# Kernel tuning notes

Measured on AMD Instinct MI355X. Metric: run time of the kernel, lower is better.

Reference implementation:

```python
import jax, jax.numpy as jnp
import numpy as np

DIM = 768
HEADS = 12
HEAD_DIM = DIM // HEADS
SCALE = HEAD_DIM ** -0.5


def setup_inputs() -> dict:
    key = jax.random.key(0)
    k1, k2, k3, k4 = jax.random.split(key, 4)
    x = jax.random.normal(k1, (1, 4096, DIM), dtype=jnp.float32)
    # qkv: Linear(dim, 3*dim), bias=False
    W_qkv = jax.random.normal(k2, (DIM, 3 * DIM), dtype=jnp.float32) * (DIM ** -0.5)
    # proj: Linear(dim, dim) with bias
    W_proj = jax.random.normal(k3, (DIM, DIM), dtype=jnp.float32) * (DIM ** -0.5)
    b_proj = jax.random.normal(k4, (DIM,), dtype=jnp.float32) * 0.01
    return {"x": x, "W_qkv": W_qkv, "W_proj": W_proj, "b_proj": b_proj}


def reference(x, W_qkv, W_proj, b_proj):
    b, n, d = x.shape
    qkv = x @ W_qkv                                  # [b, n, 3d]
    q, k, v = jnp.split(qkv, 3, axis=-1)             # each [b, n, d]
    # split heads: [b, n, (h hd)] -> [b, h, n, hd]
    def heads(t):
        return t.reshape(b, n, HEADS, HEAD_DIM).transpose(0, 2, 1, 3)
    q, k, v = heads(q) * SCALE, heads(k), heads(v)
    sim = jnp.einsum('bhid,bhjd->bhij', q, k)        # [b, h, n, n] -- full score matrix
    attn = jax.nn.softmax(sim, axis=-1)
    out = jnp.einsum('bhij,bhjd->bhid', attn, v)     # [b, h, n, hd]
    out = out.transpose(0, 2, 1, 3).reshape(b, n, d)  # merge heads
    return out @ W_proj + b_proj
```

## Files before the change

kernel.cpp:

```cpp
#include <hip/hip_runtime.h>
#include <math.h>

#define TOKENS 4096
#define DMODEL 768
#define NHEADS 12
#define HDIM   64
#define QKV_N  2304
#define ATTN_SCALE 0.125f
#define QSCALE_LOG2E (0.125f * 1.44269504088896340736f)

typedef __attribute__((ext_vector_type(8))) short bf16x8;
typedef __attribute__((ext_vector_type(4))) float floatx4;

__device__ __forceinline__ ushort f2bf(float f) {
    union { float f; unsigned u; } cv; cv.f = f;
    unsigned u = cv.u;
    u += 0x7fffu + ((u >> 16) & 1u);
    return (ushort)(u >> 16);
}

__device__ __forceinline__ unsigned cvt_pk_bf16(float a, float b) {
    unsigned r;
    asm("v_cvt_pk_bf16_f32 %0, %1, %2" : "=v"(r) : "v"(a), "v"(b));
    return r;
}

__device__ __forceinline__ void gl2lds16(const ushort* g, ushort* l) {
    __builtin_amdgcn_global_load_lds(
        (const __attribute__((address_space(1))) void*)g,
        (__attribute__((address_space(3))) void*)l, 16, 0, 0);
}

__device__ __forceinline__ bf16x8 frag(const ushort* ls, int row, int chunk) {
    return *(const bf16x8*)(ls + row * 64 + ((chunk ^ (row & 7)) * 8));
}

__global__ __launch_bounds__(256) void cvt_bf16_kernel(
    const float* __restrict__ in, ushort* __restrict__ out, int n4)
{
    const int i = blockIdx.x * 256 + threadIdx.x;
    if (i < n4) {
        const float4 v = ((const float4*)in)[i];
        ushort4 h;
        h.x = f2bf(v.x); h.y = f2bf(v.y); h.z = f2bf(v.z); h.w = f2bf(v.w);
        ((ushort4*)out)[i] = h;
    }
}

__global__ __launch_bounds__(256) void transpose_cvt_kernel(
    const float* __restrict__ in, ushort* __restrict__ out, int R, int C)
{
    __shared__ ushort tile[32][33];
    const int tx  = threadIdx.x & 31;
    const int ty8 = threadIdx.x >> 5;
    const int c0 = blockIdx.x * 32;
    const int r0 = blockIdx.y * 32;
    #pragma unroll
    for (int p = 0; p < 4; ++p) {
        const int r = ty8 + p * 8;
        tile[r][tx] = f2bf(in[(size_t)(r0 + r) * C + c0 + tx]);
    }
    __syncthreads();
    #pragma unroll
    for (int p = 0; p < 4; ++p) {
        const int c = ty8 + p * 8;
        out[(size_t)(c0 + c) * R + r0 + tx] = tile[tx][c];
    }
}

template<int NT>
__device__ __forceinline__ void gemm_body_async(
    const ushort* __restrict__ A, const ushort* __restrict__ Bt, int K,
    int m0, int n0, floatx4 acc[4][NT], ushort* ls)
{
    ushort* lsA = ls;
    ushort* lsB = ls + 8192;

    const int tid  = threadIdx.x;
    const int lane = tid & 63;
    const int wave = tid >> 6;
    const int wm = wave >> 1, wn = wave & 1;
    const int quad = lane >> 4, l16 = lane & 15;

    const int lrow = lane >> 3;
    const int csw  = ((lane & 7) ^ lrow) * 8;

    const ushort* gA = A  + (size_t)(m0 + wave * 32 + lrow) * K + csw;
    const ushort* gB = Bt + (size_t)(n0 + wave * NT * 8 + lrow) * K + csw;
    ushort* lA = lsA + (wave * 32) * 64;
    ushort* lB = lsB + (wave * NT * 8) * 64;

    for (int k0 = 0; k0 < K; k0 += 64) {
        __syncthreads();
        #pragma unroll
        for (int p = 0; p < 4; ++p)
            gl2lds16(gA + (size_t)p * 8 * K + k0, lA + p * 8 * 64);
        #pragma unroll
        for (int p = 0; p < NT; ++p)
            gl2lds16(gB + (size_t)p * 8 * K + k0, lB + p * 8 * 64);
        __syncthreads();

        #pragma unroll
        for (int ks = 0; ks < 2; ++ks) {
            bf16x8 af[4], bfr[NT];
            #pragma unroll
            for (int mt = 0; mt < 4; ++mt)
                af[mt] = frag(lsA, wm * 64 + mt * 16 + l16, ks * 4 + quad);
            #pragma unroll
            for (int nt = 0; nt < NT; ++nt)
                bfr[nt] = frag(lsB, wn * NT * 16 + nt * 16 + l16, ks * 4 + quad);
            #pragma unroll
            for (int mt = 0; mt < 4; ++mt)
                #pragma unroll
                for (int nt = 0; nt < NT; ++nt)
                    acc[mt][nt] = __builtin_amdgcn_mfma_f32_16x16x32_bf16(
                        af[mt], bfr[nt], acc[mt][nt], 0, 0, 0);
        }
    }
}

__global__ __launch_bounds__(256) void gemm_qkv_mfma(
    const ushort* __restrict__ Xb, const ushort* __restrict__ Wt,
    ushort* __restrict__ Qb, ushort* __restrict__ Kb, ushort* __restrict__ Vt)
{
    __shared__ __align__(16) ushort ls[16384];
    const int m0 = blockIdx.y * 128;
    const int n0 = blockIdx.x * 128;

    floatx4 acc[4][4] = {};
    gemm_body_async<4>(Xb, Wt, DMODEL, m0, n0, acc, ls);

    const int tid  = threadIdx.x;
    const int lane = tid & 63;
    const int wave = tid >> 6;
    const int wm = wave >> 1, wn = wave & 1;
    const int quad = lane >> 4, l16 = lane & 15;

    if (n0 < 2 * DMODEL) {
        const float scale = (n0 < DMODEL) ? QSCALE_LOG2E : 1.0f;
        ushort* outp = (n0 < DMODEL) ? Qb : Kb;
        const int colg = (n0 < DMODEL) ? n0 : n0 - DMODEL;
        #pragma unroll
        for (int p = 0; p < 2; ++p) {
            __syncthreads();
            if (wm == p) {
                #pragma unroll
                for (int mt = 0; mt < 4; ++mt)
                    #pragma unroll
                    for (int nt = 0; nt < 4; ++nt) {
                        const int row = mt * 16 + quad * 4;
                        const int col = wn * 64 + nt * 16 + l16;
                        #pragma unroll
                        for (int r = 0; r < 4; ++r)
                            ls[(row + r) * 136 + col] = f2bf(acc[mt][nt][r] * scale);
                    }
            }
            __syncthreads();
            #pragma unroll
            for (int p2 = 0; p2 < 4; ++p2) {
                const int row = (tid >> 4) + p2 * 16;
                const int c8  = (tid & 15) * 8;
                *(uint4*)(outp + (size_t)(m0 + p * 64 + row) * DMODEL + colg + c8) =
                    *(const uint4*)(ls + row * 136 + c8);
            }
        }
    } else {
        const int hd0 = n0 - 2 * DMODEL;
        #pragma unroll
        for (int p = 0; p < 2; ++p) {
            __syncthreads();
            if (wn == p) {
                #pragma unroll
                for (int mt = 0; mt < 4; ++mt)
                    #pragma unroll
                    for (int nt = 0; nt < 4; ++nt) {
                        const int hd  = nt * 16 + l16;
                        const int tok = wm * 64 + mt * 16 + quad * 4;
                        #pragma unroll
                        for (int r = 0; r < 4; ++r)
                            ls[hd * 136 + tok + r] = f2bf(acc[mt][nt][r]);
                    }
            }
            __syncthreads();
            #pragma unroll
            for (int p2 = 0; p2 < 4; ++p2) {
                const int row = (tid >> 4) + p2 * 16;
                const int c8  = (tid & 15) * 8;
                *(uint4*)(Vt + (size_t)(hd0 + p * 64 + row) * TOKENS + m0 + c8) =
                    *(const uint4*)(ls + row * 136 + c8);
            }
        }
    }
}

__global__ __launch_bounds__(256) void gemm_proj_mfma(
    const ushort* __restrict__ Ab, const ushort* __restrict__ Wt,
    const float* __restrict__ bias, float* __restrict__ out)
{
    __shared__ __align__(16) ushort ls[12288];
    const int m0 = blockIdx.y * 128;
    const int n0 = blockIdx.x * 64;

    floatx4 acc[4][2] = {};
    gemm_body_async<2>(Ab, Wt, DMODEL, m0, n0, acc, ls);

    const int lane = threadIdx.x & 63;
    const int wave = threadIdx.x >> 6;
    const int wm = wave >> 1, wn = wave & 1;
    const int quad = lane >> 4, l16 = lane & 15;
    const int row0 = m0 + wm * 64 + quad * 4;
    const int col0 = n0 + wn * 32;

    #pragma unroll
    for (int nt = 0; nt < 2; ++nt) {
        const int col = col0 + nt * 16 + l16;
        const float bv = bias[col];
        #pragma unroll
        for (int mt = 0; mt < 4; ++mt)
            #pragma unroll
            for (int r = 0; r < 4; ++r)
                out[(size_t)(row0 + mt * 16 + r) * DMODEL + col] =
                    acc[mt][nt][r] + bv;
    }
}

__global__ __launch_bounds__(256, 2) void attn_mfma_kernel(
    const ushort* __restrict__ Qb, const ushort* __restrict__ Kb,
    const ushort* __restrict__ Vt, ushort* __restrict__ attn_out)
{
    __shared__ __align__(16) ushort lds[32768];

    const int tid  = threadIdx.x;
    const int wave = tid >> 6;
    const int lane = tid & 63;
    const int quad = lane >> 4;
    const int l16  = lane & 15;
    const int h    = blockIdx.y;
    const int i0   = blockIdx.x * 64;

    bf16x8 qf[4][2];
    #pragma unroll
    for (int jt = 0; jt < 4; ++jt) {
        const ushort* qb = Qb + (size_t)(i0 + jt * 16 + l16) * DMODEL + h * HDIM;
        qf[jt][0] = *(const bf16x8*)(qb + quad * 8);
        qf[jt][1] = *(const bf16x8*)(qb + 32 + quad * 8);
    }

    bf16x8 ones;
    #pragma unroll
    for (int i = 0; i < 8; ++i) ones[i] = (short)0x3F80;

    floatx4 O[4][4] = {};
    floatx4 Ol[4]   = {};

    const int lrow8 = lane >> 3;
    const int csw8  = ((lane & 7) ^ lrow8) * 8;
    const ushort* gK = Kb + (size_t)(wave * 32 + lrow8) * DMODEL + h * HDIM + csw8;
    const int l4 = lane >> 4;
    const ushort* gVrow = Vt + (size_t)(h * HDIM + wave * 16 + l4) * TOKENS;

    #pragma unroll
    for (int p = 0; p < 4; ++p)
        gl2lds16(gK + (size_t)p * 8 * DMODEL, lds + (wave * 32 + p * 8) * 64);
    #pragma unroll
    for (int p = 0; p < 4; ++p) {
        const int vsw = ((lane & 15) ^ (p * 4 + l4)) * 8;
        gl2lds16(gVrow + (size_t)(p * 4) * TOKENS + vsw,
                 lds + 16384 + (wave * 16 + p * 4) * 128);
    }

    for (int j0 = 0; j0 < TOKENS; j0 += 128) {
        const int cur = (j0 >> 7) & 1;
        const ushort* Ks = lds + cur * 8192;
        const ushort* Vs = lds + 16384 + cur * 8192;
        ushort* Kn = lds + (1 - cur) * 8192;
        ushort* Vn = lds + 16384 + (1 - cur) * 8192;

        __syncthreads();

        if (j0 + 128 < TOKENS) {
            #pragma unroll
            for (int p = 0; p < 4; ++p)
                gl2lds16(gK + (size_t)(j0 + 128) * DMODEL + (size_t)p * 8 * DMODEL,
                         Kn + (wave * 32 + p * 8) * 64);
            #pragma unroll
            for (int p = 0; p < 4; ++p) {
                const int vsw = ((lane & 15) ^ (p * 4 + l4)) * 8;
                gl2lds16(gVrow + (size_t)(p * 4) * TOKENS + (j0 + 128) + vsw,
                         Vn + (wave * 16 + p * 4) * 128);
            }
        }

        bf16x8 af[2][2];
        #pragma unroll
        for (int ks2 = 0; ks2 < 2; ++ks2)
            #pragma unroll
            for (int kh = 0; kh < 2; ++kh)
                af[ks2][kh] = frag(Ks, wave * 32 + ks2 * 16 + l16, kh * 4 + quad);

        bf16x8 vf[4];
        #pragma unroll
        for (int nt = 0; nt < 4; ++nt) {
            const int vrow = nt * 16 + l16;
            union { bf16x8 v; uint2 d[2]; } vu;
            #pragma unroll
            for (int ks2 = 0; ks2 < 2; ++ks2) {
                const int t   = wave * 4 + ks2 * 2 + (quad >> 1);
                const int pos = t ^ (vrow & 15);
                vu.d[ks2] = *(const uint2*)(Vs + vrow * 128 + pos * 8 + (quad & 1) * 4);
            }
            vf[nt] = vu.v;
        }

        floatx4 Sv[4][2];
        #pragma unroll
        for (int jt = 0; jt < 4; ++jt)
            #pragma unroll
            for (int ks2 = 0; ks2 < 2; ++ks2) {
                floatx4 s = {0.f, 0.f, 0.f, 0.f};
                s = __builtin_amdgcn_mfma_f32_16x16x32_bf16(af[ks2][0], qf[jt][0], s, 0, 0, 0);
                s = __builtin_amdgcn_mfma_f32_16x16x32_bf16(af[ks2][1], qf[jt][1], s, 0, 0, 0);
                Sv[jt][ks2] = s;
            }

        bf16x8 pa[4];
        #pragma unroll
        for (int jt = 0; jt < 4; ++jt) {
            union { bf16x8 v; unsigned u[4]; } pu;
            #pragma unroll
            for (int ks2 = 0; ks2 < 2; ++ks2) {
                const float p0 = __builtin_amdgcn_exp2f(Sv[jt][ks2][0]);
                const float p1 = __builtin_amdgcn_exp2f(Sv[jt][ks2][1]);
                const float p2 = __builtin_amdgcn_exp2f(Sv[jt][ks2][2]);
                const float p3 = __builtin_amdgcn_exp2f(Sv[jt][ks2][3]);
                pu.u[ks2 * 2]     = cvt_pk_bf16(p0, p1);
                pu.u[ks2 * 2 + 1] = cvt_pk_bf16(p2, p3);
            }
            pa[jt] = pu.v;
            Ol[jt] = __builtin_amdgcn_mfma_f32_16x16x32_bf16(pa[jt], ones, Ol[jt], 0, 0, 0);
        }

        #pragma unroll
        for (int jt = 0; jt < 4; ++jt)
            #pragma unroll
            for (int nt = 0; nt < 4; ++nt)
                O[jt][nt] = __builtin_amdgcn_mfma_f32_16x16x32_bf16(
                    pa[jt], vf[nt], O[jt][nt], 0, 0, 0);
    }

    __syncthreads();
    float* Of  = (float*)lds;
    float* Olf = ((float*)lds) + 3 * 64 * 66;
    if (wave != 0) {
        const int rg = (wave - 1) * 64 * 66;
        #pragma unroll
        for (int jt = 0; jt < 4; ++jt) {
            #pragma unroll
            for (int nt = 0; nt < 4; ++nt)
                #pragma unroll
                for (int r = 0; r < 4; ++r)
                    Of[rg + (jt * 16 + quad * 4 + r) * 66 + nt * 16 + l16] = O[jt][nt][r];
            if (l16 == 0) {
                #pragma unroll
                for (int r = 0; r < 4; ++r)
                    Olf[(wave - 1) * 64 + jt * 16 + quad * 4 + r] = Ol[jt][r];
            }
        }
    }
    __syncthreads();
    if (wave == 0) {
        #pragma unroll
        for (int jt = 0; jt < 4; ++jt) {
            const int qr = jt * 16 + quad * 4;
            float linv[4];
            #pragma unroll
            for (int r = 0; r < 4; ++r) {
                const float l = Ol[jt][r] + Olf[qr + r] + Olf[64 + qr + r]
                              + Olf[128 + qr + r];
                linv[r] = __builtin_amdgcn_rcpf(l);
            }
            #pragma unroll
            for (int nt = 0; nt < 4; ++nt) {
                const int d = h * HDIM + nt * 16 + l16;
                #pragma unroll
                for (int r = 0; r < 4; ++r) {
                    const float o = O[jt][nt][r]
                        + Of[(qr + r) * 66 + nt * 16 + l16]
                        + Of[64 * 66 + (qr + r) * 66 + nt * 16 + l16]
                        + Of[2 * 64 * 66 + (qr + r) * 66 + nt * 16 + l16];
                    attn_out[(size_t)(i0 + qr + r) * DMODEL + d] = f2bf(o * linv[r]);
                }
            }
        }
    }
}

extern "C" void kernel_launch(void* const* d_in, const int* in_sizes, int n_in,
                              void* d_out, int out_size, void* d_ws, size_t ws_size,
                              hipStream_t stream)
{
    const float* x     = (const float*)d_in[0];
    const float* Wqkv  = (const float*)d_in[1];
    const float* Wproj = (const float*)d_in[2];
    const float* bproj = (const float*)d_in[3];
    float* out = (float*)d_out;

    ushort* Xb     = (ushort*)d_ws;
    ushort* WqkvT  = Xb    + (size_t)TOKENS * DMODEL;
    ushort* WprojT = WqkvT + (size_t)QKV_N * DMODEL;
    ushort* Qb     = WprojT + (size_t)DMODEL * DMODEL;
    ushort* Kb     = Qb    + (size_t)TOKENS * DMODEL;
    ushort* Vt     = Kb    + (size_t)TOKENS * DMODEL;
    ushort* attn   = Vt    + (size_t)TOKENS * DMODEL;

    cvt_bf16_kernel<<<dim3(TOKENS * DMODEL / 4 / 256), 256, 0, stream>>>(
        x, Xb, TOKENS * DMODEL / 4);
    transpose_cvt_kernel<<<dim3(QKV_N / 32, DMODEL / 32), 256, 0, stream>>>(
        Wqkv, WqkvT, DMODEL, QKV_N);
    transpose_cvt_kernel<<<dim3(DMODEL / 32, DMODEL / 32), 256, 0, stream>>>(
        Wproj, WprojT, DMODEL, DMODEL);

    gemm_qkv_mfma<<<dim3(QKV_N / 128, TOKENS / 128), 256, 0, stream>>>(
        Xb, WqkvT, Qb, Kb, Vt);

    attn_mfma_kernel<<<dim3(TOKENS / 64, NHEADS), 256, 0, stream>>>(
        Qb, Kb, Vt, attn);

    gemm_proj_mfma<<<dim3(DMODEL / 64, TOKENS / 128), 256, 0, stream>>>(
        attn, WprojT, bproj, out);
}
```

Measured before the change: 216.1 us.

## Split attention waves into query and key groups, load K directly from global

Reorganizes the attention kernel so the four waves form a 2x2 grid: each pair covers 32 query rows and half of each 128-key tile, instead of every wave covering all 64 queries and a quarter of the keys. K fragments are now read straight from global memory into registers, so only V stays double-buffered in LDS. This halves LDS use, lets launch bounds ask for three blocks per CU, and shrinks the final cross-wave reduction to one partner. In exchange each K element is loaded twice per block from global/L2 without LDS staging, and the K loads now sit on the critical path with no prefetch.

```diff
diff --git a/kernel.cpp b/kernel.cpp
--- a/kernel.cpp
+++ b/kernel.cpp
@@ -224,24 +224,26 @@
     }
 }
 
-__global__ __launch_bounds__(256, 2) void attn_mfma_kernel(
+__global__ __launch_bounds__(256, 3) void attn_mfma_kernel(
     const ushort* __restrict__ Qb, const ushort* __restrict__ Kb,
     const ushort* __restrict__ Vt, ushort* __restrict__ attn_out)
 {
-    __shared__ __align__(16) ushort lds[32768];
+    __shared__ __align__(16) ushort lds[16384];
 
     const int tid  = threadIdx.x;
     const int wave = tid >> 6;
+    const int qg   = wave >> 1;
+    const int kg   = wave & 1;
     const int lane = tid & 63;
     const int quad = lane >> 4;
     const int l16  = lane & 15;
     const int h    = blockIdx.y;
     const int i0   = blockIdx.x * 64;
 
-    bf16x8 qf[4][2];
-    #pragma unroll
-    for (int jt = 0; jt < 4; ++jt) {
-        const ushort* qb = Qb + (size_t)(i0 + jt * 16 + l16) * DMODEL + h * HDIM;
+    bf16x8 qf[2][2];
+    #pragma unroll
+    for (int jt = 0; jt < 2; ++jt) {
+        const ushort* qb = Qb + (size_t)(i0 + qg * 32 + jt * 16 + l16) * DMODEL + h * HDIM;
         qf[jt][0] = *(const bf16x8*)(qb + quad * 8);
         qf[jt][1] = *(const bf16x8*)(qb + 32 + quad * 8);
     }
@@ -250,39 +252,29 @@
     #pragma unroll
     for (int i = 0; i < 8; ++i) ones[i] = (short)0x3F80;
 
-    floatx4 O[4][4] = {};
-    floatx4 Ol[4]   = {};
-
-    const int lrow8 = lane >> 3;
-    const int csw8  = ((lane & 7) ^ lrow8) * 8;
-    const ushort* gK = Kb + (size_t)(wave * 32 + lrow8) * DMODEL + h * HDIM + csw8;
-    const int l4 = lane >> 4;
+    floatx4 O[2][4] = {};
+    floatx4 Ol[2]   = {};
+
+    const ushort* gKf = Kb + (size_t)(kg * 64 + l16) * DMODEL + h * HDIM + quad * 8;
+
+    const int l4 = quad;
     const ushort* gVrow = Vt + (size_t)(h * HDIM + wave * 16 + l4) * TOKENS;
 
-    #pragma unroll
-    for (int p = 0; p < 4; ++p)
-        gl2lds16(gK + (size_t)p * 8 * DMODEL, lds + (wave * 32 + p * 8) * 64);
     #pragma unroll
     for (int p = 0; p < 4; ++p) {
         const int vsw = ((lane & 15) ^ (p * 4 + l4)) * 8;
         gl2lds16(gVrow + (size_t)(p * 4) * TOKENS + vsw,
-                 lds + 16384 + (wave * 16 + p * 4) * 128);
+                 lds + (wave * 16 + p * 4) * 128);
     }
 
     for (int j0 = 0; j0 < TOKENS; j0 += 128) {
         const int cur = (j0 >> 7) & 1;
-        const ushort* Ks = lds + cur * 8192;
-        const ushort* Vs = lds + 16384 + cur * 8192;
-        ushort* Kn = lds + (1 - cur) * 8192;
-        ushort* Vn = lds + 16384 + (1 - cur) * 8192;
+        const ushort* Vs = lds + cur * 8192;
+        ushort* Vn = lds + (1 - cur) * 8192;
 
         __syncthreads();
 
         if (j0 + 128 < TOKENS) {
-            #pragma unroll
-            for (int p = 0; p < 4; ++p)
-                gl2lds16(gK + (size_t)(j0 + 128) * DMODEL + (size_t)p * 8 * DMODEL,
-                         Kn + (wave * 32 + p * 8) * 64);
             #pragma unroll
             for (int p = 0; p < 4; ++p) {
                 const int vsw = ((lane & 15) ^ (p * 4 + l4)) * 8;
@@ -291,92 +283,92 @@
             }
         }
 
-        bf16x8 af[2][2];
-        #pragma unroll
-        for (int ks2 = 0; ks2 < 2; ++ks2)
-            #pragma unroll
-            for (int kh = 0; kh < 2; ++kh)
-                af[ks2][kh] = frag(Ks, wave * 32 + ks2 * 16 + l16, kh * 4 + quad);
-
-        bf16x8 vf[4];
-        #pragma unroll
-        for (int nt = 0; nt < 4; ++nt) {
-            const int vrow = nt * 16 + l16;
-            union { bf16x8 v; uint2 d[2]; } vu;
-            #pragma unroll
-            for (int ks2 = 0; ks2 < 2; ++ks2) {
-                const int t   = wave * 4 + ks2 * 2 + (quad >> 1);
-                const int pos = t ^ (vrow & 15);
-                vu.d[ks2] = *(const uint2*)(Vs + vrow * 128 + pos * 8 + (quad & 1) * 4);
-            }
-            vf[nt] = vu.v;
-        }
-
-        floatx4 Sv[4][2];
-        #pragma unroll
-        for (int jt = 0; jt < 4; ++jt)
-            #pragma unroll
-            for (int ks2 = 0; ks2 < 2; ++ks2) {
-                floatx4 s = {0.f, 0.f, 0.f, 0.f};
-                s = __builtin_amdgcn_mfma_f32_16x16x32_bf16(af[ks2][0], qf[jt][0], s, 0, 0, 0);
-                s = __builtin_amdgcn_mfma_f32_16x16x32_bf16(af[ks2][1], qf[jt][1], s, 0, 0, 0);
-                Sv[jt][ks2] = s;
-            }
-
-        bf16x8 pa[4];
-        #pragma unroll
-        for (int jt = 0; jt < 4; ++jt) {
-            union { bf16x8 v; unsigned u[4]; } pu;
-            #pragma unroll
-            for (int ks2 = 0; ks2 < 2; ++ks2) {
-                const float p0 = __builtin_amdgcn_exp2f(Sv[jt][ks2][0]);
-                const float p1 = __builtin_amdgcn_exp2f(Sv[jt][ks2][1]);
-                const float p2 = __builtin_amdgcn_exp2f(Sv[jt][ks2][2]);
-                const float p3 = __builtin_amdgcn_exp2f(Sv[jt][ks2][3]);
-                pu.u[ks2 * 2]     = cvt_pk_bf16(p0, p1);
-                pu.u[ks2 * 2 + 1] = cvt_pk_bf16(p2, p3);
-            }
-            pa[jt] = pu.v;
-            Ol[jt] = __builtin_amdgcn_mfma_f32_16x16x32_bf16(pa[jt], ones, Ol[jt], 0, 0, 0);
-        }
-
-        #pragma unroll
-        for (int jt = 0; jt < 4; ++jt)
-            #pragma unroll
-            for (int nt = 0; nt < 4; ++nt)
-                O[jt][nt] = __builtin_amdgcn_mfma_f32_16x16x32_bf16(
-                    pa[jt], vf[nt], O[jt][nt], 0, 0, 0);
+        bf16x8 pa[2][2];
+        #pragma unroll
+        for (int g = 0; g < 2; ++g) {
+            bf16x8 af[2][2];
+            #pragma unroll
+            for (int kt2 = 0; kt2 < 2; ++kt2)
+                #pragma unroll
+                for (int kh = 0; kh < 2; ++kh)
+                    af[kt2][kh] = *(const bf16x8*)(
+                        gKf + (size_t)(j0 + g * 32 + kt2 * 16) * DMODEL + kh * 32);
+
+            floatx4 sv[2][2];
+            #pragma unroll
+            for (int jt = 0; jt < 2; ++jt)
+                #pragma unroll
+                for (int kt2 = 0; kt2 < 2; ++kt2) {
+                    floatx4 s = {0.f, 0.f, 0.f, 0.f};
+                    s = __builtin_amdgcn_mfma_f32_16x16x32_bf16(af[kt2][0], qf[jt][0], s, 0, 0, 0);
+                    s = __builtin_amdgcn_mfma_f32_16x16x32_bf16(af[kt2][1], qf[jt][1], s, 0, 0, 0);
+                    sv[jt][kt2] = s;
+                }
+
+            #pragma unroll
+            for (int jt = 0; jt < 2; ++jt) {
+                union { bf16x8 v; unsigned u[4]; } pu;
+                #pragma unroll
+                for (int h2 = 0; h2 < 2; ++h2) {
+                    const float p0 = __builtin_amdgcn_exp2f(sv[jt][h2][0]);
+                    const float p1 = __builtin_amdgcn_exp2f(sv[jt][h2][1]);
+                    const float p2 = __builtin_amdgcn_exp2f(sv[jt][h2][2]);
+                    const float p3 = __builtin_amdgcn_exp2f(sv[jt][h2][3]);
+                    pu.u[h2 * 2]     = cvt_pk_bf16(p0, p1);
+                    pu.u[h2 * 2 + 1] = cvt_pk_bf16(p2, p3);
+                }
+                pa[g][jt] = pu.v;
+                Ol[jt] = __builtin_amdgcn_mfma_f32_16x16x32_bf16(pa[g][jt], ones, Ol[jt], 0, 0, 0);
+            }
+        }
+
+        #pragma unroll
+        for (int g = 0; g < 2; ++g)
+            #pragma unroll
+            for (int nt = 0; nt < 4; ++nt) {
+                const int vrow = nt * 16 + l16;
+                union { bf16x8 v; uint2 d[2]; } vu;
+                #pragma unroll
+                for (int h2 = 0; h2 < 2; ++h2) {
+                    const int t   = kg * 8 + g * 4 + h2 * 2 + (quad >> 1);
+                    const int pos = t ^ l16;
+                    vu.d[h2] = *(const uint2*)(Vs + vrow * 128 + pos * 8 + (quad & 1) * 4);
+                }
+                #pragma unroll
+                for (int jt = 0; jt < 2; ++jt)
+                    O[jt][nt] = __builtin_amdgcn_mfma_f32_16x16x32_bf16(
+                        pa[g][jt], vu.v, O[jt][nt], 0, 0, 0);
+            }
     }
 
     __syncthreads();
     float* Of  = (float*)lds;
-    float* Olf = ((float*)lds) + 3 * 64 * 66;
-    if (wave != 0) {
-        const int rg = (wave - 1) * 64 * 66;
-        #pragma unroll
-        for (int jt = 0; jt < 4; ++jt) {
+    float* Olf = ((float*)lds) + 2 * 32 * 66;
+    if (kg == 1) {
+        float* o = Of + qg * 32 * 66;
+        #pragma unroll
+        for (int jt = 0; jt < 2; ++jt) {
             #pragma unroll
             for (int nt = 0; nt < 4; ++nt)
                 #pragma unroll
                 for (int r = 0; r < 4; ++r)
-                    Of[rg + (jt * 16 + quad * 4 + r) * 66 + nt * 16 + l16] = O[jt][nt][r];
+                    o[(jt * 16 + quad * 4 + r) * 66 + nt * 16 + l16] = O[jt][nt][r];
             if (l16 == 0) {
                 #pragma unroll
                 for (int r = 0; r < 4; ++r)
-                    Olf[(wave - 1) * 64 + jt * 16 + quad * 4 + r] = Ol[jt][r];
+                    Olf[qg * 32 + jt * 16 + quad * 4 + r] = Ol[jt][r];
             }
         }
     }
     __syncthreads();
-    if (wave == 0) {
-        #pragma unroll
-        for (int jt = 0; jt < 4; ++jt) {
+    if (kg == 0) {
+        #pragma unroll
+        for (int jt = 0; jt < 2; ++jt) {
             const int qr = jt * 16 + quad * 4;
             float linv[4];
             #pragma unroll
             for (int r = 0; r < 4; ++r) {
-                const float l = Ol[jt][r] + Olf[qr + r] + Olf[64 + qr + r]
-                              + Olf[128 + qr + r];
+                const float l = Ol[jt][r] + Olf[qg * 32 + qr + r];
                 linv[r] = __builtin_amdgcn_rcpf(l);
             }
             #pragma unroll
@@ -385,10 +377,9 @@
                 #pragma unroll
                 for (int r = 0; r < 4; ++r) {
                     const float o = O[jt][nt][r]
-                        + Of[(qr + r) * 66 + nt * 16 + l16]
-                        + Of[64 * 66 + (qr + r) * 66 + nt * 16 + l16]
-                        + Of[2 * 64 * 66 + (qr + r) * 66 + nt * 16 + l16];
-                    attn_out[(size_t)(i0 + qr + r) * DMODEL + d] = f2bf(o * linv[r]);
+                        + Of[qg * 32 * 66 + (qr + r) * 66 + nt * 16 + l16];
+                    attn_out[(size_t)(i0 + qg * 32 + qr + r) * DMODEL + d] =
+                        f2bf(o * linv[r]);
                 }
             }
         }
```

Result: slower. 236.5 us (+9.4%).

## Give each wave private double-buffered K/V LDS tiles and drop per-iteration block barriers

Applied to the files above, without the earlier changes.

Each wave now loads only its own 32-key slice of K and V into a private LDS region, double-buffered. It waits on its own loads with s_waitcnt vmcnt instead of a block-wide __syncthreads every iteration. The V tile layout and swizzle are reworked for the smaller per-wave tile. s_setprio is raised around the MFMA sections to favour matrix issue across waves. This removes the per-tile block synchronisation and lets waves run decoupled, but the hand-written vmcnt counts must exactly match the number of issued loads to stay correct.

```diff
diff --git a/kernel.cpp b/kernel.cpp
--- a/kernel.cpp
+++ b/kernel.cpp
@@ -253,99 +253,102 @@
     floatx4 O[4][4] = {};
     floatx4 Ol[4]   = {};
 
+    ushort* wls = lds + wave * 8192;
+
     const int lrow8 = lane >> 3;
     const int csw8  = ((lane & 7) ^ lrow8) * 8;
     const ushort* gK = Kb + (size_t)(wave * 32 + lrow8) * DMODEL + h * HDIM + csw8;
-    const int l4 = lane >> 4;
-    const ushort* gVrow = Vt + (size_t)(h * HDIM + wave * 16 + l4) * TOKENS;
+
+    const int vrow4 = lane >> 2;
+    const int vslot = (lane & 3) ^ (vrow4 & 3);
+    const ushort* gV = Vt + (size_t)(h * HDIM + vrow4) * TOKENS + wave * 32 + vslot * 8;
+
+    const int vx = l16 & 3;
+    const int vo0 = (((quad >> 1)    ) ^ vx) * 8 + (quad & 1) * 4;
+    const int vo1 = ((2 + (quad >> 1)) ^ vx) * 8 + (quad & 1) * 4;
 
     #pragma unroll
     for (int p = 0; p < 4; ++p)
-        gl2lds16(gK + (size_t)p * 8 * DMODEL, lds + (wave * 32 + p * 8) * 64);
-    #pragma unroll
-    for (int p = 0; p < 4; ++p) {
-        const int vsw = ((lane & 15) ^ (p * 4 + l4)) * 8;
-        gl2lds16(gVrow + (size_t)(p * 4) * TOKENS + vsw,
-                 lds + 16384 + (wave * 16 + p * 4) * 128);
-    }
-
-    for (int j0 = 0; j0 < TOKENS; j0 += 128) {
-        const int cur = (j0 >> 7) & 1;
-        const ushort* Ks = lds + cur * 8192;
-        const ushort* Vs = lds + 16384 + cur * 8192;
-        ushort* Kn = lds + (1 - cur) * 8192;
-        ushort* Vn = lds + 16384 + (1 - cur) * 8192;
-
-        __syncthreads();
-
-        if (j0 + 128 < TOKENS) {
+        gl2lds16(gK + (size_t)p * 8 * DMODEL, wls + p * 512);
+    #pragma unroll
+    for (int p = 0; p < 4; ++p)
+        gl2lds16(gV + (size_t)p * 16 * TOKENS, wls + 2048 + p * 512);
+
+    for (int t = 0; t < TOKENS / 128; ++t) {
+        const int cur = t & 1;
+        const ushort* Kc = wls + cur * 4096;
+        const ushort* Vc = Kc + 2048;
+
+        if (t < TOKENS / 128 - 1) {
+            ushort* Kn = wls + (1 - cur) * 4096;
+            const size_t jn = (size_t)(t + 1) * 128;
             #pragma unroll
             for (int p = 0; p < 4; ++p)
-                gl2lds16(gK + (size_t)(j0 + 128) * DMODEL + (size_t)p * 8 * DMODEL,
-                         Kn + (wave * 32 + p * 8) * 64);
-            #pragma unroll
-            for (int p = 0; p < 4; ++p) {
-                const int vsw = ((lane & 15) ^ (p * 4 + l4)) * 8;
-                gl2lds16(gVrow + (size_t)(p * 4) * TOKENS + (j0 + 128) + vsw,
-                         Vn + (wave * 16 + p * 4) * 128);
-            }
-        }
+                gl2lds16(gK + (jn + p * 8) * DMODEL, Kn + p * 512);
+            #pragma unroll
+            for (int p = 0; p < 4; ++p)
+                gl2lds16(gV + (size_t)p * 16 * TOKENS + jn, Kn + 2048 + p * 512);
+            asm volatile("s_waitcnt vmcnt(8)" ::: "memory");
+        } else {
+            asm volatile("s_waitcnt vmcnt(0)" ::: "memory");
+        }
+        __builtin_amdgcn_sched_barrier(0);
 
         bf16x8 af[2][2];
         #pragma unroll
-        for (int ks2 = 0; ks2 < 2; ++ks2)
+        for (int kt2 = 0; kt2 < 2; ++kt2)
             #pragma unroll
             for (int kh = 0; kh < 2; ++kh)
-                af[ks2][kh] = frag(Ks, wave * 32 + ks2 * 16 + l16, kh * 4 + quad);
+                af[kt2][kh] = frag(Kc, kt2 * 16 + l16, kh * 4 + quad);
 
         bf16x8 vf[4];
         #pragma unroll
         for (int nt = 0; nt < 4; ++nt) {
-            const int vrow = nt * 16 + l16;
+            const ushort* vb = Vc + (nt * 16 + l16) * 32;
             union { bf16x8 v; uint2 d[2]; } vu;
-            #pragma unroll
-            for (int ks2 = 0; ks2 < 2; ++ks2) {
-                const int t   = wave * 4 + ks2 * 2 + (quad >> 1);
-                const int pos = t ^ (vrow & 15);
-                vu.d[ks2] = *(const uint2*)(Vs + vrow * 128 + pos * 8 + (quad & 1) * 4);
-            }
+            vu.d[0] = *(const uint2*)(vb + vo0);
+            vu.d[1] = *(const uint2*)(vb + vo1);
             vf[nt] = vu.v;
         }
 
         floatx4 Sv[4][2];
+        __builtin_amdgcn_s_setprio(1);
         #pragma unroll
         for (int jt = 0; jt < 4; ++jt)
             #pragma unroll
-            for (int ks2 = 0; ks2 < 2; ++ks2) {
+            for (int kt2 = 0; kt2 < 2; ++kt2) {
                 floatx4 s = {0.f, 0.f, 0.f, 0.f};
-                s = __builtin_amdgcn_mfma_f32_16x16x32_bf16(af[ks2][0], qf[jt][0], s, 0, 0, 0);
-                s = __builtin_amdgcn_mfma_f32_16x16x32_bf16(af[ks2][1], qf[jt][1], s, 0, 0, 0);
-                Sv[jt][ks2] = s;
-            }
+                s = __builtin_amdgcn_mfma_f32_16x16x32_bf16(af[kt2][0], qf[jt][0], s, 0, 0, 0);
+                s = __builtin_amdgcn_mfma_f32_16x16x32_bf16(af[kt2][1], qf[jt][1], s, 0, 0, 0);
+                Sv[jt][kt2] = s;
+            }
+        __builtin_amdgcn_s_setprio(0);
 
         bf16x8 pa[4];
         #pragma unroll
         for (int jt = 0; jt < 4; ++jt) {
             union { bf16x8 v; unsigned u[4]; } pu;
             #pragma unroll
-            for (int ks2 = 0; ks2 < 2; ++ks2) {
-                const float p0 = __builtin_amdgcn_exp2f(Sv[jt][ks2][0]);
-                const float p1 = __builtin_amdgcn_exp2f(Sv[jt][ks2][1]);
-                const float p2 = __builtin_amdgcn_exp2f(Sv[jt][ks2][2]);
-                const float p3 = __builtin_amdgcn_exp2f(Sv[jt][ks2][3]);
-                pu.u[ks2 * 2]     = cvt_pk_bf16(p0, p1);
-                pu.u[ks2 * 2 + 1] = cvt_pk_bf16(p2, p3);
+            for (int kt2 = 0; kt2 < 2; ++kt2) {
+                const float p0 = __builtin_amdgcn_exp2f(Sv[jt][kt2][0]);
+                const float p1 = __builtin_amdgcn_exp2f(Sv[jt][kt2][1]);
+                const float p2 = __builtin_amdgcn_exp2f(Sv[jt][kt2][2]);
+                const float p3 = __builtin_amdgcn_exp2f(Sv[jt][kt2][3]);
+                pu.u[kt2 * 2]     = cvt_pk_bf16(p0, p1);
+                pu.u[kt2 * 2 + 1] = cvt_pk_bf16(p2, p3);
             }
             pa[jt] = pu.v;
             Ol[jt] = __builtin_amdgcn_mfma_f32_16x16x32_bf16(pa[jt], ones, Ol[jt], 0, 0, 0);
         }
 
+        __builtin_amdgcn_s_setprio(1);
         #pragma unroll
         for (int jt = 0; jt < 4; ++jt)
             #pragma unroll
             for (int nt = 0; nt < 4; ++nt)
                 O[jt][nt] = __builtin_amdgcn_mfma_f32_16x16x32_bf16(
                     pa[jt], vf[nt], O[jt][nt], 0, 0, 0);
+        __builtin_amdgcn_s_setprio(0);
     }
 
     __syncthreads();
```

Result: faster. 208.3 us (-3.6%).
